# Performance work log

Hardware: AMD Instinct MI355X
Metric: run time of the kernel (lower is better)

The kernel has to match this reference:

```python
import jax, jax.numpy as jnp
import numpy as np

B, N, D, E_PER, NT, ET, L = 32, 64, 128, 512, 32, 16, 6
E = B * E_PER


def _ln(y, g, b, eps=1e-5):
    m = jnp.mean(y, -1, keepdims=True)
    v = jnp.mean((y - m) ** 2, -1, keepdims=True)
    return (y - m) * jax.lax.rsqrt(v + eps) * g + b


def setup_inputs() -> dict:
    key = jax.random.key(0)
    ks = jax.random.split(key, 40)
    x = jax.random.randint(ks[0], (B * N,), 0, NT)
    src = jax.random.randint(ks[1], (E,), 0, N)
    dst = jax.random.randint(ks[2], (E,), 0, N)
    off = jnp.repeat(jnp.arange(B) * N, E_PER)
    edge_index = jnp.stack([src + off, dst + off])
    edge_attr = jax.random.randint(ks[3], (E,), 0, ET)
    t = jax.random.uniform(ks[4], (B,))

    def lin(k, fi, fo):
        return jax.random.normal(k, (fi, fo), jnp.float32) / np.sqrt(fi).astype(np.float32)

    inp = {
        'x': x, 'edge_index': edge_index, 'edge_attr': edge_attr, 't': t,
        'node_emb': (jax.random.normal(ks[5], (NT, D)) * 0.02).at[0].set(0.0),
        'edge_emb': (jax.random.normal(ks[6], (ET, D)) * 0.02).at[0].set(0.0),
        'temb_W1': lin(ks[7], 1, D), 'temb_b1': jnp.zeros(D),
        'temb_W2': lin(ks[8], D, D), 'temb_b2': jnp.zeros(D),
        'nin_W1': lin(ks[9], D, 2 * D), 'nin_b1': jnp.zeros(2 * D),
        'nin_W2': lin(ks[10], 2 * D, D), 'nin_b2': jnp.zeros(D),
        'ein_W1': lin(ks[11], D, 2 * D), 'ein_b1': jnp.zeros(2 * D),
        'ein_W2': lin(ks[12], 2 * D, D), 'ein_b2': jnp.zeros(D),
        'conv_W1': jax.random.normal(ks[13], (L, 3 * D, D)) / np.sqrt(3 * D).astype(np.float32),
        'conv_b1': jnp.zeros((L, D)),
        'conv_g1': jnp.ones((L, D)), 'conv_bt1': jnp.zeros((L, D)),
        'conv_W2': jax.random.normal(ks[14], (L, D, D)) / np.sqrt(D).astype(np.float32),
        'conv_b2': jnp.zeros((L, D)),
        'conv_g2': jnp.ones((L, D)), 'conv_bt2': jnp.zeros((L, D)),
        'mlp_W1': lin(ks[15], D, D), 'mlp_b1': jnp.zeros(D),
        'mlp_W2': lin(ks[16], D, D), 'mlp_b2': jnp.zeros(D),
        'fn_W1': lin(ks[17], D, 2 * D), 'fn_b1': jnp.zeros(2 * D),
        'fn_W2': lin(ks[18], 2 * D, D), 'fn_b2': jnp.zeros(D),
    }
    return inp


def reference(x, edge_index, edge_attr, t, node_emb, edge_emb,
              temb_W1, temb_b1, temb_W2, temb_b2,
              nin_W1, nin_b1, nin_W2, nin_b2,
              ein_W1, ein_b1, ein_W2, ein_b2,
              conv_W1, conv_b1, conv_g1, conv_bt1,
              conv_W2, conv_b2, conv_g2, conv_bt2,
              mlp_W1, mlp_b1, mlp_W2, mlp_b2,
              fn_W1, fn_b1, fn_W2, fn_b2):
    silu, relu = jax.nn.silu, jax.nn.relu
    # encoders
    h = node_emb[x]                                   # (B*N, D)
    e = edge_emb[edge_attr]                           # (E, D)
    h = relu(h @ nin_W1 + nin_b1) @ nin_W2 + nin_b2
    e = relu(e @ ein_W1 + ein_b1) @ ein_W2 + ein_b2
    # densify (to_dense_adj sums duplicate edges)
    g = edge_index[0] // N
    u = edge_index[0] % N
    v = edge_index[1] % N
    adj = jnp.zeros((B, N, N, D), h.dtype).at[g, u, v].add(e)
    # time embedding scales adj
    tt = silu(silu(t[:, None] @ temb_W1 + temb_b1) @ temb_W2 + temb_b2)  # (B, D)
    X = adj * tt[:, None, None, :]
    A = X  # A fixed to initial masked tensor, X updated residually
    for l in range(L):
        X1 = jnp.einsum('bikd,bkjd->bijd', A, X)      # aggregate over dim 1
        X2 = jnp.einsum('bikd,bkjd->bijd', X, A)      # aggregate over dim 2
        y = jnp.concatenate([X, X1, X2], -1)          # (B,N,N,3D)
        y = relu(_ln(y @ conv_W1[l] + conv_b1[l], conv_g1[l], conv_bt1[l]))
        y = relu(_ln(y @ conv_W2[l] + conv_b2[l], conv_g2[l], conv_bt2[l]))
        X = X + y                                     # residual, samesparse add
    X = X + jnp.transpose(X, (0, 2, 1, 3))
    e_out = X[g, u, v]                                # (E, D) edge gather
    h2 = (silu(X @ mlp_W1 + mlp_b1) @ mlp_W2 + mlp_b2).mean(-2).reshape(B * N, D)
    node_out = relu(h2 @ fn_W1 + fn_b1) @ fn_W2 + fn_b2
    edge_out = relu(e_out @ fn_W1 + fn_b1) @ fn_W2 + fn_b2  # original uses final_layer_node for edges too
    graph_attr = node_out.reshape(B, N, -1).mean(1)   # global mean pool
    return node_out, edge_out, graph_attr
```

## Files before the change

### kernel.cpp

```cpp
#include <hip/hip_runtime.h>
#include <hip/hip_bf16.h>
#include <math.h>

#define NB 32
#define NNODE 64
#define DD 128
#define NSQ 4096
#define EDGES 16384
#define LAYERS 6

typedef __bf16 bf16x8 __attribute__((ext_vector_type(8)));
typedef float f32x4 __attribute__((ext_vector_type(4)));

__device__ __forceinline__ float silu_f(float x){ return x / (1.f + __expf(-x)); }
__device__ __forceinline__ float bf2f(unsigned short h){
  union{unsigned int u; float f;} x; x.u = ((unsigned int)h)<<16; return x.f;
}

__global__ void k_temb(const float* __restrict__ t, const float* __restrict__ W1,
                       const float* __restrict__ b1, const float* __restrict__ W2,
                       const float* __restrict__ b2, float* __restrict__ tt){
  int b = blockIdx.x, d = threadIdx.x;
  __shared__ float h[DD];
  float v = t[b]*W1[d] + b1[d];
  h[d] = silu_f(v);
  __syncthreads();
  float acc = b2[d];
  #pragma unroll 4
  for (int k=0;k<DD;k++) acc = fmaf(h[k], W2[k*DD+d], acc);
  tt[b*DD+d] = silu_f(acc);
}

__global__ void k_edgeenc(const float* __restrict__ emb, const float* __restrict__ W1,
                          const float* __restrict__ b1, const float* __restrict__ W2,
                          const float* __restrict__ b2, float* __restrict__ enc){
  int et = blockIdx.x, tid = threadIdx.x;
  __shared__ float e0[DD];
  __shared__ float hid[2*DD];
  if (tid < DD) e0[tid] = emb[et*DD + tid];
  __syncthreads();
  float a = b1[tid];
  for (int d2=0; d2<DD; d2++) a = fmaf(e0[d2], W1[d2*256 + tid], a);
  hid[tid] = fmaxf(a, 0.f);
  __syncthreads();
  if (tid < DD){
    float o = b2[tid];
    for (int k=0;k<256;k++) o = fmaf(hid[k], W2[k*DD + tid], o);
    enc[et*DD + tid] = o;
  }
}

__global__ void k_cnt(const int* __restrict__ ei, const int* __restrict__ attr,
                      unsigned int* __restrict__ cnt, int b0){
  int e = b0*512 + blockIdx.x*256 + threadIdx.x;
  int s = ei[e], dN = ei[EDGES+e];
  int g = (s>>6) - b0, u = s&63, v = dN&63;
  atomicAdd(&cnt[((size_t)g*4096 + v*64 + u)*16 + attr[e]], 1u);
}

__global__ __launch_bounds__(256) void k_expand(const unsigned int* __restrict__ cnt,
    const float* __restrict__ enc, const float* __restrict__ tt,
    __bf16* __restrict__ A_S, int b0){
  __shared__ float encs[16][128];
  __shared__ float ttl[128];
  __shared__ __bf16 tb[8][256];
  int g = blockIdx.x >> 4;
  int cell0 = (blockIdx.x & 15) << 8;
  int tid = threadIdx.x;
  for (int s = tid; s < 2048; s += 256) encs[s>>7][s&127] = enc[s];
  if (tid < 128) ttl[tid] = tt[(b0+g)*128 + tid];
  unsigned int c16[16];
  { const uint4* src = (const uint4*)(cnt + ((size_t)g*4096 + cell0 + tid)*16);
    uint4 a = src[0], b = src[1], c = src[2], d = src[3];
    c16[0]=a.x; c16[1]=a.y; c16[2]=a.z; c16[3]=a.w;
    c16[4]=b.x; c16[5]=b.y; c16[6]=b.z; c16[7]=b.w;
    c16[8]=c.x; c16[9]=c.y; c16[10]=c.z; c16[11]=c.w;
    c16[12]=d.x; c16[13]=d.y; c16[14]=d.z; c16[15]=d.w; }
  __syncthreads();
  for (int dc=0; dc<16; dc++){
    int d0 = dc*8;
    float vals[8] = {0.f,0.f,0.f,0.f,0.f,0.f,0.f,0.f};
    #pragma unroll
    for (int et=0; et<16; et++){
      unsigned int c = c16[et];
      if (c){
        float fc = (float)c;
        #pragma unroll
        for (int dd=0; dd<8; dd++) vals[dd] = fmaf(fc, encs[et][d0+dd], vals[dd]);
      }
    }
    #pragma unroll
    for (int dd=0; dd<8; dd++) tb[dd][tid] = (__bf16)(vals[dd]*ttl[d0+dd]);
    __syncthreads();
    { int dd = tid>>5, seg = tid&31;
      uint4 v = *(const uint4*)&tb[dd][seg*8];
      *(uint4*)(A_S + ((size_t)(g*128 + d0 + dd)<<12) + cell0 + seg*8) = v; }
    __syncthreads();
  }
}

__global__ __launch_bounds__(256) void k_wprep(const float* __restrict__ W1, const float* __restrict__ W2,
                                               const float* __restrict__ Wm, __bf16* __restrict__ WT){
  int b = blockIdx.x, t = threadIdx.x;
  const float* src; __bf16* dst; int K;
  if (b < 6){ src = W1 + (size_t)b*384*128; dst = WT + (size_t)b*49152; K = 384; }
  else if (b < 12){ src = W2 + (size_t)(b-6)*128*128; dst = WT + 294912 + (size_t)(b-6)*16384; K = 128; }
  else { src = Wm; dst = WT + 393216; K = 128; }
  __shared__ float L[64][129];
  for (int k0 = 0; k0 < K; k0 += 64){
    __syncthreads();
    int r = t>>2, c = (t&3)*32;
    #pragma unroll
    for (int e=0;e<32;e+=4){
      float4 x = *(const float4*)(src + (size_t)(k0+r)*128 + c + e);
      L[r][c+e]=x.x; L[r][c+e+1]=x.y; L[r][c+e+2]=x.z; L[r][c+e+3]=x.w;
    }
    __syncthreads();
    int fo = t>>1, kk = (t&1)*32;
    union { __bf16 h[32]; uint4 u[4]; } o;
    #pragma unroll
    for (int e=0;e<32;e++) o.h[e] = (__bf16)L[kk+e][fo];
    uint4* d4 = (uint4*)(dst + (size_t)fo*K + k0 + kk);
    d4[0]=o.u[0]; d4[1]=o.u[1]; d4[2]=o.u[2]; d4[3]=o.u[3];
  }
}

__global__ __launch_bounds__(256) void k_wprepfn(const float* __restrict__ W1, const float* __restrict__ W2,
                                                 __bf16* __restrict__ o1, __bf16* __restrict__ o2){
  int b = blockIdx.x, t = threadIdx.x;
  const float* src; __bf16* dst; int K, N, k0, n0;
  if (b < 8){ src = W1; dst = o1; K = 128; N = 256; k0 = (b>>2)*64; n0 = (b&3)*64; }
  else { int bb = b-8; src = W2; dst = o2; K = 256; N = 128; k0 = (bb>>1)*64; n0 = (bb&1)*64; }
  __shared__ float L[64][65];
  int r = t>>2, c4 = (t&3)*16;
  #pragma unroll
  for (int e=0;e<16;e+=4){
    float4 x = *(const float4*)(src + (size_t)(k0+r)*N + n0 + c4 + e);
    L[r][c4+e]=x.x; L[r][c4+e+1]=x.y; L[r][c4+e+2]=x.z; L[r][c4+e+3]=x.w;
  }
  __syncthreads();
  int n = t>>2, kc = (t&3)*16;
  union { __bf16 h[16]; uint4 u[2]; } o;
  #pragma unroll
  for (int e=0;e<16;e++) o.h[e] = (__bf16)L[kc+e][n];
  uint4* d4 = (uint4*)(dst + (size_t)(n0+n)*K + k0 + kc);
  d4[0]=o.u[0]; d4[1]=o.u[1];
}

__global__ __launch_bounds__(256) void k_einsum(const __bf16* __restrict__ As,
                                                const __bf16* __restrict__ Xs,
                                                __bf16* __restrict__ X1t, __bf16* __restrict__ X2t){
  __shared__ __bf16 S[8][4096];
  int tid = threadIdx.x;
  size_t p0 = (size_t)blockIdx.x * 2;
  #pragma unroll
  for (int k2 = 0; k2 < 4; k2++){
    int slot = (k2 < 2) ? (2 + k2) : (4 + k2);
    const __bf16* srcp = (k2 < 2) ? As : Xs;
    const uint4* g = (const uint4*)(srcp + (p0 + (k2&1))*4096);
    #pragma unroll
    for (int s = 0; s < 2; s++){
      int idx = tid + s*256;
      uint4 v = g[idx];
      int row = idx>>3, slt = idx&7;
      *(uint4*)&S[slot][row*64 + ((slt ^ (row&7))<<3)] = v;
    }
  }
  __syncthreads();
  {
    int q = tid>>6, v = tid&63;
    int ssl = (q<2) ? (2+q) : (4+q);
    int dsl = (q<2) ? q : (2+q);
    const unsigned char* sb = (const unsigned char*)S[ssl];
    unsigned char* db = (unsigned char*)S[dsl];
    #pragma unroll
    for (int uo=0; uo<8; uo++){
      union { __bf16 h[8]; uint4 u; } pk;
      #pragma unroll
      for (int e=0;e<8;e++){
        int u = uo*8+e;
        pk.h[e] = *(const __bf16*)(sb + u*128 + (((v>>3) ^ (u&7))<<4) + (v&7)*2);
      }
      *(uint4*)(db + v*128 + ((uo ^ (v&7))<<4)) = pk.u;
    }
  }
  __syncthreads();
  int w = tid>>6, lane = tid&63;
  int pl = w>>1, pr = w&1;
  const __bf16* M  = pr ? S[4+pl] : S[0+pl];
  const __bf16* Bt = pr ? S[2+pl] : S[6+pl];
  f32x4 acc[4][4];
  #pragma unroll
  for (int a=0;a<4;a++)
    #pragma unroll
    for(int b=0;b<4;b++) acc[a][b] = (f32x4){0.f,0.f,0.f,0.f};
  int lr = lane&15, lq = lane>>4;
  #pragma unroll
  for (int ks=0;ks<2;ks++){
    bf16x8 af[4], bfr[4];
    #pragma unroll
    for (int mt=0;mt<4;mt++){ int r = mt*16+lr; af[mt] = *(const bf16x8*)&M[r*64 + (((ks*4+lq) ^ (r&7))<<3)]; }
    #pragma unroll
    for (int nt=0;nt<4;nt++){ int r = nt*16+lr; bfr[nt] = *(const bf16x8*)&Bt[r*64 + (((ks*4+lq) ^ (r&7))<<3)]; }
    #pragma unroll
    for (int mt=0;mt<4;mt++)
      #pragma unroll
      for (int nt=0;nt<4;nt++)
        acc[mt][nt] = __builtin_amdgcn_mfma_f32_16x16x32_bf16(af[mt], bfr[nt], acc[mt][nt], 0,0,0);
  }
  __bf16* OUT = (pr ? X2t : X1t) + (p0+pl)*4096;
  #pragma unroll
  for (int mt=0;mt<4;mt++)
    #pragma unroll
    for (int nt=0;nt<4;nt++){
      int col = nt*16 + lr; int row0 = mt*16 + lq*4;
      union { __bf16 h[4]; uint2 u; } o;
      #pragma unroll
      for (int r=0;r<4;r++) o.h[r] = (__bf16)acc[mt][nt][r];
      *(uint2*)&OUT[col*64 + row0] = o.u;
    }
}

__global__ __launch_bounds__(256) void k_layer(const __bf16* __restrict__ Xold,
    const __bf16* __restrict__ X1, const __bf16* __restrict__ X2,
    const __bf16* __restrict__ W1t, const __bf16* __restrict__ W2t,
    const float* __restrict__ b1v, const float* __restrict__ g1v, const float* __restrict__ bt1v,
    const float* __restrict__ b2v, const float* __restrict__ g2v, const float* __restrict__ bt2v,
    __bf16* __restrict__ Xnew){
  __shared__ __align__(16) unsigned char WcB[8192];
  __shared__ __align__(16) unsigned char RG[32768];
  __bf16* Wc = (__bf16*)WcB;
  unsigned char* Nc = RG;
  unsigned char* Cc = RG + 8192;
  __bf16* y1T = (__bf16*)RG;
  float (*redS)[128] = (float(*)[128])(RG + 16384);
  float (*redQ)[128] = (float(*)[128])(RG + 18432);
  float (*stats)[128] = (float(*)[128])WcB;
  int tid = threadIdx.x, w = tid>>6, lane = tid&63, lr = lane&15, lq = lane>>4;
  int colTile = blockIdx.x << 7;
  int bl = colTile >> 12;
  int colInB = colTile & 4095;
  f32x4 acc[2][8];
  #pragma unroll
  for (int a=0;a<2;a++)
    #pragma unroll
    for (int b=0;b<8;b++) acc[a][b] = (f32x4){0.f,0.f,0.f,0.f};

  for (int ks=0; ks<12; ks++){
    __syncthreads();
    { int fo = tid>>1, half = tid&1;
      const uint4* src = (const uint4*)(W1t + (size_t)fo*384 + ks*32 + half*16);
      uint4 v0 = src[0], v1 = src[1];
      *(uint4*)&Wc[fo*32 + (((half*2+0) ^ (fo&3))<<3)] = v0;
      *(uint4*)&Wc[fo*32 + (((half*2+1) ^ (fo&3))<<3)] = v1;
    }
    { int fi = tid>>3, o = tid&7;
      int gfi = ks*32 + fi;
      const __bf16* T = (gfi<128)? Xold : (gfi<256? X1 : X2);
      int d = gfi & 127;
      const uint4* src = (const uint4*)(T + ((size_t)(bl*128 + d)<<12) + colInB + o*16);
      uint4 v0 = src[0], v1 = src[1];
      *(uint4*)(Nc + fi*256 + (((o*2+0) ^ (fi&15))<<4)) = v0;
      *(uint4*)(Nc + fi*256 + (((o*2+1) ^ (fi&15))<<4)) = v1;
    }
    __syncthreads();
    { int col = tid>>1;
      #pragma unroll
      for (int j=0;j<2;j++){
        int oct = (tid&1)*2 + j;
        union { __bf16 h[8]; uint4 u; } pk;
        #pragma unroll
        for (int e=0;e<8;e++){
          int fi = oct*8 + e;
          pk.h[e] = *(const __bf16*)(Nc + fi*256 + (((col>>3) ^ (fi&15))<<4) + (col&7)*2);
        }
        *(uint4*)(Cc + col*64 + ((oct ^ (col&3))<<4)) = pk.u;
      }
    }
    __syncthreads();
    bf16x8 af[2], bfr[8];
    #pragma unroll
    for (int mt=0;mt<2;mt++){ int fo = w*32+mt*16+lr; af[mt] = *(const bf16x8*)&Wc[fo*32 + ((lq ^ (fo&3))<<3)]; }
    #pragma unroll
    for (int nt=0;nt<8;nt++){ int cr = nt*16+lr; bfr[nt] = *(const bf16x8*)(Cc + cr*64 + ((lq ^ (cr&3))<<4)); }
    #pragma unroll
    for (int mt=0;mt<2;mt++)
      #pragma unroll
      for (int nt=0;nt<8;nt++)
        acc[mt][nt] = __builtin_amdgcn_mfma_f32_16x16x32_bf16(af[mt], bfr[nt], acc[mt][nt], 0,0,0);
  }

  #pragma unroll
  for (int mt=0;mt<2;mt++){
    #pragma unroll
    for (int r=0;r<4;r++){
      float bv = b1v[w*32 + mt*16 + lq*4 + r];
      #pragma unroll
      for (int nt=0;nt<8;nt++) acc[mt][nt][r] += bv;
    }
  }
  {
    float cs[8], cq[8];
    #pragma unroll
    for (int nt=0;nt<8;nt++){ cs[nt]=0.f; cq[nt]=0.f; }
    #pragma unroll
    for (int mt=0;mt<2;mt++)
      #pragma unroll
      for (int nt=0;nt<8;nt++)
        #pragma unroll
        for (int r=0;r<4;r++){ float v = acc[mt][nt][r]; cs[nt] += v; cq[nt] = fmaf(v,v,cq[nt]); }
    #pragma unroll
    for (int nt=0;nt<8;nt++){
      cs[nt] += __shfl_xor(cs[nt], 16); cq[nt] += __shfl_xor(cq[nt], 16);
      cs[nt] += __shfl_xor(cs[nt], 32); cq[nt] += __shfl_xor(cq[nt], 32);
    }
    if (lq == 0){
      #pragma unroll
      for (int nt=0;nt<8;nt++){ redS[w][nt*16+lr] = cs[nt]; redQ[w][nt*16+lr] = cq[nt]; }
    }
  }
  __syncthreads();
  if (tid < 128){
    float S = redS[0][tid]+redS[1][tid]+redS[2][tid]+redS[3][tid];
    float Q = redQ[0][tid]+redQ[1][tid]+redQ[2][tid]+redQ[3][tid];
    float m = S*(1.f/128.f);
    float var = Q*(1.f/128.f) - m*m;
    stats[0][tid] = m; stats[1][tid] = rsqrtf(var + 1e-5f);
  }
  __syncthreads();
  #pragma unroll
  for (int mt=0;mt<2;mt++){
    int fo1b = w*32 + mt*16 + lq*4;
    float ga[4], be[4];
    #pragma unroll
    for (int r=0;r<4;r++){ ga[r] = g1v[fo1b+r]; be[r] = bt1v[fo1b+r]; }
    #pragma unroll
    for (int nt=0;nt<8;nt++){
      int col = nt*16 + lr;
      union { __bf16 h[4]; uint2 u; } o;
      #pragma unroll
      for (int r=0;r<4;r++){
        float xx = (acc[mt][nt][r] - stats[0][col]) * stats[1][col] * ga[r] + be[r];
        o.h[r] = (__bf16)fmaxf(xx, 0.f);
      }
      *(uint2*)&y1T[col*128 + (fo1b ^ ((col&15)<<3))] = o.u;
    }
  }
  __syncthreads();

  f32x4 acc2[2][8];
  #pragma unroll
  for (int a=0;a<2;a++)
    #pragma unroll
    for (int b=0;b<8;b++) acc2[a][b] = (f32x4){0.f,0.f,0.f,0.f};
  for (int ks2=0; ks2<4; ks2++){
    if (ks2) __syncthreads();
    { int fo = tid>>1, half = tid&1;
      const uint4* src = (const uint4*)(W2t + (size_t)fo*128 + ks2*32 + half*16);
      uint4 v0 = src[0], v1 = src[1];
      *(uint4*)&Wc[fo*32 + (((half*2+0) ^ (fo&3))<<3)] = v0;
      *(uint4*)&Wc[fo*32 + (((half*2+1) ^ (fo&3))<<3)] = v1;
    }
    __syncthreads();
    bf16x8 af[2], bfr[8];
    #pragma unroll
    for (int mt=0;mt<2;mt++){ int fo = w*32+mt*16+lr; af[mt] = *(const bf16x8*)&Wc[fo*32 + ((lq ^ (fo&3))<<3)]; }
    #pragma unroll
    for (int nt=0;nt<8;nt++){ int cr = nt*16+lr; bfr[nt] = *(const bf16x8*)&y1T[cr*128 + ((ks2*32 + lq*8) ^ ((cr&15)<<3))]; }
    #pragma unroll
    for (int mt=0;mt<2;mt++)
      #pragma unroll
      for (int nt=0;nt<8;nt++)
        acc2[mt][nt] = __builtin_amdgcn_mfma_f32_16x16x32_bf16(af[mt], bfr[nt], acc2[mt][nt], 0,0,0);
  }
  __syncthreads();

  #pragma unroll
  for (int mt=0;mt<2;mt++){
    #pragma unroll
    for (int r=0;r<4;r++){
      float bv = b2v[w*32 + mt*16 + lq*4 + r];
      #pragma unroll
      for (int nt=0;nt<8;nt++) acc2[mt][nt][r] += bv;
    }
  }
  {
    float cs[8], cq[8];
    #pragma unroll
    for (int nt=0;nt<8;nt++){ cs[nt]=0.f; cq[nt]=0.f; }
    #pragma unroll
    for (int mt=0;mt<2;mt++)
      #pragma unroll
      for (int nt=0;nt<8;nt++)
        #pragma unroll
        for (int r=0;r<4;r++){ float v = acc2[mt][nt][r]; cs[nt] += v; cq[nt] = fmaf(v,v,cq[nt]); }
    #pragma unroll
    for (int nt=0;nt<8;nt++){
      cs[nt] += __shfl_xor(cs[nt], 16); cq[nt] += __shfl_xor(cq[nt], 16);
      cs[nt] += __shfl_xor(cs[nt], 32); cq[nt] += __shfl_xor(cq[nt], 32);
    }
    if (lq == 0){
      #pragma unroll
      for (int nt=0;nt<8;nt++){ redS[w][nt*16+lr] = cs[nt]; redQ[w][nt*16+lr] = cq[nt]; }
    }
  }
  __syncthreads();
  if (tid < 128){
    float S = redS[0][tid]+redS[1][tid]+redS[2][tid]+redS[3][tid];
    float Q = redQ[0][tid]+redQ[1][tid]+redQ[2][tid]+redQ[3][tid];
    float m = S*(1.f/128.f);
    float var = Q*(1.f/128.f) - m*m;
    stats[0][tid] = m; stats[1][tid] = rsqrtf(var + 1e-5f);
  }
  __syncthreads();
  #pragma unroll
  for (int mt=0;mt<2;mt++){
    #pragma unroll
    for (int r=0;r<4;r++){
      int fo = w*32 + mt*16 + lq*4 + r;
      float ga = g2v[fo], be = bt2v[fo];
      size_t rowb = ((size_t)(bl*128 + fo)<<12) + colInB;
      #pragma unroll
      for (int nt=0;nt<8;nt++){
        int cp = nt*16 + lr;
        float xx = (acc2[mt][nt][r] - stats[0][cp]) * stats[1][cp] * ga + be;
        float o = fmaxf(xx, 0.f);
        float old = (float)Xold[rowb + cp];
        Xnew[rowb + cp] = (__bf16)(o + old);
      }
    }
  }
}

__global__ __launch_bounds__(256) void k_sym(const __bf16* __restrict__ Xin, __bf16* __restrict__ Xout){
  __shared__ float P[64][65];
  size_t base = (size_t)blockIdx.x * 4096;
  int tid = threadIdx.x;
  int f = tid*16, r = f>>6, c = f&63;
  union { __bf16 h[16]; uint4 u[2]; } in;
  in.u[0] = *(const uint4*)(Xin + base + f);
  in.u[1] = *(const uint4*)(Xin + base + f + 8);
  #pragma unroll
  for (int e=0;e<16;e++) P[r][c+e] = (float)in.h[e];
  __syncthreads();
  union { __bf16 h[16]; uint4 u[2]; } o;
  #pragma unroll
  for (int e=0;e<16;e++) o.h[e] = (__bf16)(P[r][c+e] + P[c+e][r]);
  *(uint4*)(Xout + base + f)     = o.u[0];
  *(uint4*)(Xout + base + f + 8) = o.u[1];
}

__global__ __launch_bounds__(256) void k_tonm(const __bf16* __restrict__ S, __bf16* __restrict__ NM){
  __shared__ unsigned short L[64][65];
  int b = blockIdx.x;
  int g = b >> 7, dh = (b>>6)&1, cc = b&63;
  int cell0 = cc*64, d0 = dh*64;
  int tid = threadIdx.x;
  int r = tid>>2, c = (tid&3)*16;
  union { unsigned short h[16]; uint4 u[2]; } in;
  const unsigned short* src = (const unsigned short*)S + ((size_t)(g*128 + d0 + r)<<12) + cell0 + c;
  in.u[0] = *(const uint4*)src;
  in.u[1] = *(const uint4*)(src + 8);
  #pragma unroll
  for (int e=0;e<16;e++) L[r][c+e] = in.h[e];
  __syncthreads();
  union { unsigned short h[16]; uint4 u[2]; } o;
  int cr = tid>>2, dc = (tid&3)*16;
  #pragma unroll
  for (int e=0;e<16;e++) o.h[e] = L[dc+e][cr];
  unsigned short* dst = (unsigned short*)NM + (size_t)(g*4096 + cell0 + cr)*128 + d0 + dc;
  *(uint4*)dst       = o.u[0];
  *(uint4*)(dst + 8) = o.u[1];
}

__global__ __launch_bounds__(256) void k_mlph(const __bf16* __restrict__ NM,
    const __bf16* __restrict__ Wt, const float* __restrict__ bias, __bf16* __restrict__ hid){
  __shared__ __align__(16) unsigned char WcB[8192];
  __shared__ __align__(16) unsigned char EcB[8192];
  __bf16* Wc = (__bf16*)WcB;
  unsigned char* Ec = EcB;
  int tid = threadIdx.x, w = tid>>6, lane = tid&63, lr = lane&15, lq = lane>>4;
  int g = blockIdx.x >> 5;
  size_t cellbase = ((size_t)g<<12) + ((size_t)(blockIdx.x & 31) << 7);
  int mh = w&1, nh = w>>1;
  f32x4 acc[4][4];
  #pragma unroll
  for (int a=0;a<4;a++)
    #pragma unroll
    for (int b=0;b<4;b++) acc[a][b] = (f32x4){0.f,0.f,0.f,0.f};
  for (int ks=0; ks<4; ks++){
    __syncthreads();
    { int fo = tid>>1, half = tid&1;
      const uint4* src = (const uint4*)(Wt + (size_t)fo*128 + ks*32 + half*16);
      uint4 v0 = src[0], v1 = src[1];
      *(uint4*)&Wc[fo*32 + (((half*2+0) ^ (fo&3))<<3)] = v0;
      *(uint4*)&Wc[fo*32 + (((half*2+1) ^ (fo&3))<<3)] = v1;
    }
    { int cell = tid>>1, half = tid&1;
      const uint4* src = (const uint4*)(NM + (cellbase + cell)*128 + ks*32 + half*16);
      uint4 v0 = src[0], v1 = src[1];
      *(uint4*)(Ec + cell*64 + (((half*2+0) ^ (cell&3))<<4)) = v0;
      *(uint4*)(Ec + cell*64 + (((half*2+1) ^ (cell&3))<<4)) = v1;
    }
    __syncthreads();
    bf16x8 af[4], bfr[4];
    #pragma unroll
    for (int mt=0;mt<4;mt++){ int cr = mh*64 + mt*16 + lr; af[mt] = *(const bf16x8*)(Ec + cr*64 + ((lq ^ (cr&3))<<4)); }
    #pragma unroll
    for (int nt=0;nt<4;nt++){ int fo = nh*64 + nt*16 + lr; bfr[nt] = *(const bf16x8*)&Wc[fo*32 + ((lq ^ (fo&3))<<3)]; }
    #pragma unroll
    for (int mt=0;mt<4;mt++)
      #pragma unroll
      for (int nt=0;nt<4;nt++)
        acc[mt][nt] = __builtin_amdgcn_mfma_f32_16x16x32_bf16(af[mt], bfr[nt], acc[mt][nt], 0,0,0);
  }
  #pragma unroll
  for (int mt=0;mt<4;mt++)
    #pragma unroll
    for (int r=0;r<4;r++){
      size_t cell = cellbase + mh*64 + mt*16 + lq*4 + r;
      #pragma unroll
      for (int nt=0;nt<4;nt++){
        int fo = nh*64 + nt*16 + lr;
        hid[cell*128 + fo] = (__bf16)silu_f(acc[mt][nt][r] + bias[fo]);
      }
    }
}

__global__ void k_ymean(const __bf16* __restrict__ hid, float* __restrict__ ym){
  __shared__ float red[256];
  int g = blockIdx.x >> 6, u = blockIdx.x & 63;
  int fo = threadIdx.x & 127, vh = threadIdx.x >> 7;
  const unsigned short* hu = (const unsigned short*)hid;
  float s = 0.f;
  for (int v = vh; v < 64; v += 2)
    s += bf2f(hu[((size_t)g*4096 + v*64 + u)*128 + fo]);
  red[threadIdx.x] = s;
  __syncthreads();
  if (vh == 0) ym[((size_t)g*64 + u)*128 + fo] = (red[fo] + red[128+fo]) * (1.f/64.f);
}

__global__ void k_h2(const float* __restrict__ ym, const float* __restrict__ W2,
                     const float* __restrict__ b2, float* __restrict__ h2){
  int row = blockIdx.x, fo = threadIdx.x;
  __shared__ float rr[128];
  rr[fo] = ym[(size_t)row*128 + fo];
  __syncthreads();
  float a = b2[fo];
  #pragma unroll 4
  for (int k=0;k<128;k++) a = fmaf(rr[k], W2[k*128+fo], a);
  h2[(size_t)row*128+fo] = a;
}

template<int GATHER>
__global__ __launch_bounds__(256) void k_fmlp(const __bf16* __restrict__ NM, const float* __restrict__ RWS,
    const int* __restrict__ ei,
    const __bf16* __restrict__ W1t, const float* __restrict__ b1,
    const __bf16* __restrict__ W2t, const float* __restrict__ b2,
    float* __restrict__ outp, int b0){
  __shared__ __align__(16) unsigned char RA[32768];
  __shared__ __align__(16) unsigned char RB[8192];
  __shared__ int cells[64];
  __bf16* eo  = (__bf16*)RA;
  __bf16* Wc  = (__bf16*)(RA + 16384);
  __bf16* hid = (__bf16*)RA;
  __bf16* W2c = (__bf16*)RB;
  int tid = threadIdx.x, w = tid>>6, lane = tid&63, lr = lane&15, lq = lane>>4;
  int r0 = blockIdx.x*64;
  if (GATHER){
    if (tid < 64){
      int e = b0*512 + r0 + tid;
      int s = ei[e], dN = ei[EDGES+e];
      cells[tid] = ((s>>6) - b0)*4096 + (dN&63)*64 + (s&63);
    }
    __syncthreads();
  }
  { int el = tid>>2, o4 = tid&3;
    if (GATHER){
      const unsigned short* src = (const unsigned short*)NM + (size_t)cells[el]*128;
      #pragma unroll
      for (int j=0;j<4;j++){
        int ch = o4*4 + j;
        uint4 v = *(const uint4*)(src + ch*8);
        *(uint4*)&eo[el*128 + ((ch*8) ^ ((el&15)*8))] = v;
      }
    } else {
      const float* src = RWS + (size_t)(r0 + el)*128;
      #pragma unroll
      for (int j=0;j<4;j++){
        int ch = o4*4 + j;
        union { __bf16 h[8]; uint4 u; } pk;
        #pragma unroll
        for (int e2=0;e2<8;e2++) pk.h[e2] = (__bf16)src[ch*8 + e2];
        *(uint4*)&eo[el*128 + ((ch*8) ^ ((el&15)*8))] = pk.u;
      }
    }
  }
  f32x4 acc[4][4];
  #pragma unroll
  for (int a=0;a<4;a++)
    #pragma unroll
    for (int b=0;b<4;b++) acc[a][b] = (f32x4){0.f,0.f,0.f,0.f};
  for (int ks=0; ks<4; ks++){
    if (ks) __syncthreads();
    { int fo = tid;
      const uint4* src = (const uint4*)(W1t + (size_t)fo*128 + ks*32);
      #pragma unroll
      for (int o=0;o<4;o++){
        uint4 v = src[o];
        *(uint4*)&Wc[fo*32 + ((o ^ (fo&3))<<3)] = v;
      }
    }
    __syncthreads();
    bf16x8 af[4], bfr[4];
    #pragma unroll
    for (int mt=0;mt<4;mt++){ int fo = w*64+mt*16+lr; af[mt] = *(const bf16x8*)&Wc[fo*32 + ((lq ^ (fo&3))<<3)]; }
    #pragma unroll
    for (int nt=0;nt<4;nt++){ int ed = nt*16+lr; bfr[nt] = *(const bf16x8*)&eo[ed*128 + ((ks*32+lq*8) ^ ((ed&15)*8))]; }
    #pragma unroll
    for (int mt=0;mt<4;mt++)
      #pragma unroll
      for (int nt=0;nt<4;nt++)
        acc[mt][nt] = __builtin_amdgcn_mfma_f32_16x16x32_bf16(af[mt], bfr[nt], acc[mt][nt], 0,0,0);
  }
  __syncthreads();
  #pragma unroll
  for (int mt=0;mt<4;mt++){
    int fob = w*64 + mt*16 + lq*4;
    float bv[4];
    #pragma unroll
    for (int r=0;r<4;r++) bv[r] = b1[fob+r];
    #pragma unroll
    for (int nt=0;nt<4;nt++){
      int ed = nt*16 + lr;
      union { __bf16 h[4]; uint2 u; } o;
      #pragma unroll
      for (int r=0;r<4;r++) o.h[r] = (__bf16)fmaxf(acc[mt][nt][r] + bv[r], 0.f);
      *(uint2*)&hid[ed*256 + (fob ^ ((ed&31)*8))] = o.u;
    }
  }
  f32x4 acc2[4][2];
  #pragma unroll
  for (int a=0;a<4;a++)
    #pragma unroll
    for (int b=0;b<2;b++) acc2[a][b] = (f32x4){0.f,0.f,0.f,0.f};
  int mh = w&1, nh = w>>1;
  for (int ks2=0; ks2<8; ks2++){
    __syncthreads();
    { int fo = tid>>1, half = tid&1;
      const uint4* src = (const uint4*)(W2t + (size_t)fo*256 + ks2*32 + half*16);
      uint4 v0 = src[0], v1 = src[1];
      *(uint4*)&W2c[fo*32 + (((half*2+0) ^ (fo&3))<<3)] = v0;
      *(uint4*)&W2c[fo*32 + (((half*2+1) ^ (fo&3))<<3)] = v1;
    }
    __syncthreads();
    bf16x8 af2[4], bfr2[2];
    #pragma unroll
    for (int mt=0;mt<4;mt++){ int fo2 = mh*64+mt*16+lr; af2[mt] = *(const bf16x8*)&W2c[fo2*32 + ((lq ^ (fo2&3))<<3)]; }
    #pragma unroll
    for (int nt=0;nt<2;nt++){ int ed = nh*32+nt*16+lr; bfr2[nt] = *(const bf16x8*)&hid[ed*256 + ((ks2*32+lq*8) ^ ((ed&31)*8))]; }
    #pragma unroll
    for (int mt=0;mt<4;mt++)
      #pragma unroll
      for (int nt=0;nt<2;nt++)
        acc2[mt][nt] = __builtin_amdgcn_mfma_f32_16x16x32_bf16(af2[mt], bfr2[nt], acc2[mt][nt], 0,0,0);
  }
  #pragma unroll
  for (int mt=0;mt<4;mt++){
    int fo2b = mh*64 + mt*16 + lq*4;
    float bv[4];
    #pragma unroll
    for (int r=0;r<4;r++) bv[r] = b2[fo2b+r];
    #pragma unroll
    for (int nt=0;nt<2;nt++){
      int ed = nh*32 + nt*16 + lr;
      float4 o = make_float4(acc2[mt][nt][0]+bv[0], acc2[mt][nt][1]+bv[1],
                             acc2[mt][nt][2]+bv[2], acc2[mt][nt][3]+bv[3]);
      *(float4*)(outp + (size_t)(r0 + ed)*128 + fo2b) = o;
    }
  }
}

__global__ void k_graph(const float* __restrict__ node_out, float* __restrict__ gout){
  int b = blockIdx.x, d = threadIdx.x;
  float s = 0.f;
  for (int i=0;i<64;i++) s += node_out[(size_t)(b*64+i)*128 + d];
  gout[b*128 + d] = s * (1.f/64.f);
}

extern "C" void kernel_launch(void* const* d_in, const int* in_sizes, int n_in,
                              void* d_out, int out_size, void* d_ws, size_t ws_size,
                              hipStream_t stream) {
  const int*   edge_index = (const int*)d_in[1];
  const int*   edge_attr  = (const int*)d_in[2];
  const float* t        = (const float*)d_in[3];
  const float* edge_emb = (const float*)d_in[5];
  const float* temb_W1  = (const float*)d_in[6];
  const float* temb_b1  = (const float*)d_in[7];
  const float* temb_W2  = (const float*)d_in[8];
  const float* temb_b2  = (const float*)d_in[9];
  const float* ein_W1   = (const float*)d_in[14];
  const float* ein_b1   = (const float*)d_in[15];
  const float* ein_W2   = (const float*)d_in[16];
  const float* ein_b2   = (const float*)d_in[17];
  const float* conv_W1  = (const float*)d_in[18];
  const float* conv_b1  = (const float*)d_in[19];
  const float* conv_g1  = (const float*)d_in[20];
  const float* conv_bt1 = (const float*)d_in[21];
  const float* conv_W2  = (const float*)d_in[22];
  const float* conv_b2  = (const float*)d_in[23];
  const float* conv_g2  = (const float*)d_in[24];
  const float* conv_bt2 = (const float*)d_in[25];
  const float* mlp_W1   = (const float*)d_in[26];
  const float* mlp_b1   = (const float*)d_in[27];
  const float* mlp_W2   = (const float*)d_in[28];
  const float* mlp_b2   = (const float*)d_in[29];
  const float* fn_W1    = (const float*)d_in[30];
  const float* fn_b1    = (const float*)d_in[31];
  const float* fn_W2    = (const float*)d_in[32];
  const float* fn_b2    = (const float*)d_in[33];

  float* ws  = (float*)d_ws;
  float* tt  = ws;
  float* enc = ws + 4096;
  float* ym  = ws + 6144;
  float* h2  = ws + 268288;
  __bf16* WT = (__bf16*)(ws + 530432);
  unsigned int* cnt = (unsigned int*)(ws + 768000);
  const size_t HDRF = 2883584;

  __bf16* fnW1t = WT + 409600;
  __bf16* fnW2t = WT + 442368;

  size_t availF = ws_size / sizeof(float);
  const int cands[6] = {32, 16, 8, 4, 2, 1};
  int C = 1;
  for (int i = 0; i < 6; i++){
    if (HDRF + 4ull * (size_t)cands[i] * 262144ull <= availF){ C = cands[i]; break; }
  }
  const size_t PCB = (size_t)C * 262144;
  __bf16* A_S = (__bf16*)(ws + HDRF);
  __bf16* X_S = (__bf16*)(ws + HDRF + PCB);
  __bf16* X1  = (__bf16*)(ws + HDRF + 2*PCB);
  __bf16* X2  = (__bf16*)(ws + HDRF + 3*PCB);
  float* outf = (float*)d_out;

  k_temb<<<NB, DD, 0, stream>>>(t, temb_W1, temb_b1, temb_W2, temb_b2, tt);
  k_edgeenc<<<16, 256, 0, stream>>>(edge_emb, ein_W1, ein_b1, ein_W2, ein_b2, enc);
  k_wprep<<<13, 256, 0, stream>>>(conv_W1, conv_W2, mlp_W1, WT);
  k_wprepfn<<<16, 256, 0, stream>>>(fn_W1, fn_W2, fnW1t, fnW2t);

  for (int b0 = 0; b0 < NB; b0 += C){
    hipMemsetAsync(cnt, 0, (size_t)C*4096*16*sizeof(unsigned int), stream);
    k_cnt<<<C*2, 256, 0, stream>>>(edge_index, edge_attr, cnt, b0);
    k_expand<<<C*16, 256, 0, stream>>>(cnt, enc, tt, A_S, b0);

    for (int l=0; l<LAYERS; l++){
      const __bf16* Xs_l = (l==0) ? A_S : X_S;
      k_einsum<<<C*64, 256, 0, stream>>>(A_S, Xs_l, X1, X2);
      k_layer<<<C*32, 256, 0, stream>>>(Xs_l, X1, X2,
          WT + (size_t)l*49152, WT + 294912 + (size_t)l*16384,
          conv_b1 + l*DD, conv_g1 + l*DD, conv_bt1 + l*DD,
          conv_b2 + l*DD, conv_g2 + l*DD, conv_bt2 + l*DD, X_S);
    }

    k_sym<<<C*128, 256, 0, stream>>>(X_S, X2);
    k_tonm<<<C*128, 256, 0, stream>>>(X2, X1);
    k_mlph<<<C*32, 256, 0, stream>>>(X1, WT + 393216, mlp_b1, X2);
    k_ymean<<<C*64, 256, 0, stream>>>(X2, ym);
    k_h2<<<C*64, 128, 0, stream>>>(ym, mlp_W2, mlp_b2, h2);
    k_fmlp<1><<<C*8, 256, 0, stream>>>(X1, nullptr, edge_index, fnW1t, fn_b1, fnW2t, fn_b2,
                                       outf + 262144 + (size_t)b0*512*128, b0);
    k_fmlp<0><<<C, 256, 0, stream>>>(nullptr, h2, nullptr, fnW1t, fn_b1, fnW2t, fn_b2,
                                     outf + (size_t)b0*64*128, b0);
    k_graph<<<C, DD, 0, stream>>>(outf + (size_t)b0*64*DD, outf + 2359296 + b0*DD);
  }
}
```

Before: 655.4 us.

## Use direct global-to-LDS loads and LDS-staged coalesced stores in einsum and layer kernels

```diff
diff --git a/kernel.cpp b/kernel.cpp
--- a/kernel.cpp
+++ b/kernel.cpp
@@ -11,6 +11,12 @@
 
 typedef __bf16 bf16x8 __attribute__((ext_vector_type(8)));
 typedef float f32x4 __attribute__((ext_vector_type(4)));
+
+typedef __attribute__((address_space(1))) const unsigned int g_u32;
+typedef __attribute__((address_space(3))) unsigned int l_u32;
+__device__ __forceinline__ void gll16(const void* g, void* l){
+  __builtin_amdgcn_global_load_lds((g_u32*)g, (l_u32*)l, 16, 0, 0);
+}
 
 __device__ __forceinline__ float silu_f(float x){ return x / (1.f + __expf(-x)); }
 __device__ __forceinline__ float bf2f(unsigned short h){
@@ -152,18 +158,16 @@
                                                 __bf16* __restrict__ X1t, __bf16* __restrict__ X2t){
   __shared__ __bf16 S[8][4096];
   int tid = threadIdx.x;
+  int w = tid>>6, lane = tid&63;
   size_t p0 = (size_t)blockIdx.x * 2;
-  #pragma unroll
-  for (int k2 = 0; k2 < 4; k2++){
-    int slot = (k2 < 2) ? (2 + k2) : (4 + k2);
-    const __bf16* srcp = (k2 < 2) ? As : Xs;
-    const uint4* g = (const uint4*)(srcp + (p0 + (k2&1))*4096);
-    #pragma unroll
-    for (int s = 0; s < 2; s++){
-      int idx = tid + s*256;
-      uint4 v = g[idx];
-      int row = idx>>3, slt = idx&7;
-      *(uint4*)&S[slot][row*64 + ((slt ^ (row&7))<<3)] = v;
+  {
+    int slot = (w<2) ? (2+w) : (4+w);
+    const __bf16* srcp = ((w<2) ? As : Xs) + (p0 + (w&1))*4096;
+    #pragma unroll
+    for (int c8 = 0; c8 < 8; c8++){
+      int row = c8*8 + (lane>>3);
+      int ch  = (lane&7) ^ (row&7);
+      gll16(srcp + row*64 + ch*8, (char*)&S[slot][0] + c8*1024);
     }
   }
   __syncthreads();
@@ -185,7 +189,6 @@
     }
   }
   __syncthreads();
-  int w = tid>>6, lane = tid&63;
   int pl = w>>1, pr = w&1;
   const __bf16* M  = pr ? S[4+pl] : S[0+pl];
   const __bf16* Bt = pr ? S[2+pl] : S[6+pl];
@@ -208,17 +211,35 @@
       for (int nt=0;nt<4;nt++)
         acc[mt][nt] = __builtin_amdgcn_mfma_f32_16x16x32_bf16(af[mt], bfr[nt], acc[mt][nt], 0,0,0);
   }
-  __bf16* OUT = (pr ? X2t : X1t) + (p0+pl)*4096;
-  #pragma unroll
-  for (int mt=0;mt<4;mt++)
-    #pragma unroll
-    for (int nt=0;nt<4;nt++){
-      int col = nt*16 + lr; int row0 = mt*16 + lq*4;
-      union { __bf16 h[4]; uint2 u; } o;
-      #pragma unroll
-      for (int r=0;r<4;r++) o.h[r] = (__bf16)acc[mt][nt][r];
-      *(uint2*)&OUT[col*64 + row0] = o.u;
-    }
+  {
+    int dslot = pr ? (4+pl) : pl;
+    unsigned char* db = (unsigned char*)&S[dslot][0];
+    #pragma unroll
+    for (int mt=0;mt<4;mt++)
+      #pragma unroll
+      for (int nt=0;nt<4;nt++){
+        int col = nt*16 + lr; int row0 = mt*16 + lq*4;
+        union { __bf16 h[4]; uint2 u; } o;
+        #pragma unroll
+        for (int r=0;r<4;r++) o.h[r] = (__bf16)acc[mt][nt][r];
+        int chunk = row0>>3;
+        *(uint2*)(db + col*128 + ((chunk ^ (col&7))<<4) + (row0&7)*2) = o.u;
+      }
+  }
+  __syncthreads();
+  #pragma unroll
+  for (int s4=0; s4<4; s4++){
+    int slot = (s4<2) ? s4 : (2+s4);
+    __bf16* dst = ((s4<2) ? X1t : X2t) + (p0 + (s4&1))*4096;
+    const unsigned char* sb = (const unsigned char*)&S[slot][0];
+    #pragma unroll
+    for (int q=0;q<2;q++){
+      int t2 = tid + q*256;
+      int col = t2>>3, rc = t2&7;
+      uint4 v = *(const uint4*)(sb + col*128 + ((rc ^ (col&7))<<4));
+      *(uint4*)(dst + t2*8) = v;
+    }
+  }
 }
 
 __global__ __launch_bounds__(256) void k_layer(const __bf16* __restrict__ Xold,
@@ -248,23 +269,30 @@
 
   for (int ks=0; ks<12; ks++){
     __syncthreads();
-    { int fo = tid>>1, half = tid&1;
-      const uint4* src = (const uint4*)(W1t + (size_t)fo*384 + ks*32 + half*16);
-      uint4 v0 = src[0], v1 = src[1];
-      *(uint4*)&Wc[fo*32 + (((half*2+0) ^ (fo&3))<<3)] = v0;
-      *(uint4*)&Wc[fo*32 + (((half*2+1) ^ (fo&3))<<3)] = v1;
-    }
-    { int fi = tid>>3, o = tid&7;
-      int gfi = ks*32 + fi;
-      const __bf16* T = (gfi<128)? Xold : (gfi<256? X1 : X2);
-      int d = gfi & 127;
-      const uint4* src = (const uint4*)(T + ((size_t)(bl*128 + d)<<12) + colInB + o*16);
-      uint4 v0 = src[0], v1 = src[1];
-      *(uint4*)(Nc + fi*256 + (((o*2+0) ^ (fi&15))<<4)) = v0;
-      *(uint4*)(Nc + fi*256 + (((o*2+1) ^ (fi&15))<<4)) = v1;
-    }
-    __syncthreads();
-    { int col = tid>>1;
+    {
+      #pragma unroll
+      for (int cw=0; cw<2; cw++){
+        int fo = (w*2+cw)*16 + (lane>>2);
+        int c4 = lane&3;
+        gll16(W1t + (size_t)fo*384 + ks*32 + ((c4 ^ (fo&3))<<3),
+              (char*)WcB + (w*2+cw)*1024);
+      }
+    }
+    {
+      #pragma unroll
+      for (int cn=0; cn<2; cn++){
+        int fi = (w*2+cn)*4 + (lane>>4);
+        int c16 = lane&15;
+        int gfi = ks*32 + fi;
+        const __bf16* T = (gfi<128)? Xold : (gfi<256? X1 : X2);
+        int d = gfi & 127;
+        gll16(T + ((size_t)(bl*128 + d)<<12) + colInB + ((c16 ^ (fi&15))<<3),
+              (char*)RG + (w*2+cn)*1024);
+      }
+    }
+    __syncthreads();
+    {
+      int col = tid>>1;
       #pragma unroll
       for (int j=0;j<2;j++){
         int oct = (tid&1)*2 + j;
@@ -355,11 +383,14 @@
     for (int b=0;b<8;b++) acc2[a][b] = (f32x4){0.f,0.f,0.f,0.f};
   for (int ks2=0; ks2<4; ks2++){
     if (ks2) __syncthreads();
-    { int fo = tid>>1, half = tid&1;
-      const uint4* src = (const uint4*)(W2t + (size_t)fo*128 + ks2*32 + half*16);
-      uint4 v0 = src[0], v1 = src[1];
-      *(uint4*)&Wc[fo*32 + (((half*2+0) ^ (fo&3))<<3)] = v0;
-      *(uint4*)&Wc[fo*32 + (((half*2+1) ^ (fo&3))<<3)] = v1;
+    {
+      #pragma unroll
+      for (int cw=0; cw<2; cw++){
+        int fo = (w*2+cw)*16 + (lane>>2);
+        int c4 = lane&3;
+        gll16(W2t + (size_t)fo*128 + ks2*32 + ((c4 ^ (fo&3))<<3),
+              (char*)WcB + (w*2+cw)*1024);
+      }
     }
     __syncthreads();
     bf16x8 af[2], bfr[8];
@@ -419,15 +450,31 @@
     for (int r=0;r<4;r++){
       int fo = w*32 + mt*16 + lq*4 + r;
       float ga = g2v[fo], be = bt2v[fo];
-      size_t rowb = ((size_t)(bl*128 + fo)<<12) + colInB;
       #pragma unroll
       for (int nt=0;nt<8;nt++){
         int cp = nt*16 + lr;
         float xx = (acc2[mt][nt][r] - stats[0][cp]) * stats[1][cp] * ga + be;
-        float o = fmaxf(xx, 0.f);
-        float old = (float)Xold[rowb + cp];
-        Xnew[rowb + cp] = (__bf16)(o + old);
-      }
+        int ch = cp>>3;
+        int swz = (ch & 8) | ((ch ^ (fo&7)) & 7);
+        *(__bf16*)(RG + fo*256 + (swz<<4) + (cp&7)*2) = (__bf16)fmaxf(xx, 0.f);
+      }
+    }
+  }
+  __syncthreads();
+  {
+    int row = tid>>1, half = tid&1;
+    size_t gb = ((size_t)(bl*128 + row)<<12) + colInB + half*64;
+    #pragma unroll
+    for (int j=0;j<8;j++){
+      int ch = half*8 + j;
+      int swz = (ch & 8) | ((ch ^ (row&7)) & 7);
+      uint4 tv = *(const uint4*)(RG + row*256 + (swz<<4));
+      uint4 ov = *(const uint4*)(Xold + gb + j*8);
+      union { __bf16 h[8]; uint4 u; } a, b, o;
+      a.u = tv; b.u = ov;
+      #pragma unroll
+      for (int e=0;e<8;e++) o.h[e] = (__bf16)((float)a.h[e] + (float)b.h[e]);
+      *(uint4*)(Xnew + gb + j*8) = o.u;
     }
   }
 }
```

After: 645.8 us. No clear change (-1.5%).
